# Kernel optimization log

Measured on AMD Instinct MI355X. Metric: run time of the kernel, lower is better.

Reference implementation:

```python
import jax, jax.numpy as jnp
import numpy as np

N = 100000      # nodes
E = 1600000     # edges (before self-loops)
IN = 256        # input features
HID = 128       # hidden channels
HEADS = 8
C = HID // HEADS  # per-head channels = 16
L = 3           # num GAT layers
EPS = 1e-5      # batchnorm eps
NEG_SLOPE = 0.2 # leaky relu slope (PyG GATConv default)


def setup_inputs() -> dict:
    key = jax.random.key(0)
    ks = jax.random.split(key, 8)
    s = 0.05
    x = jax.random.normal(ks[0], (N, IN), jnp.float32)
    edge_index = jax.random.randint(ks[1], (2, E), 0, N, dtype=jnp.int32)
    proj_w = jax.random.normal(ks[2], (IN, HID), jnp.float32) * s
    proj_b = jnp.zeros((HID,), jnp.float32)
    W = jax.random.normal(ks[3], (L, HID, HID), jnp.float32) * s
    att_src = jax.random.normal(ks[4], (L, HEADS, C), jnp.float32) * s
    att_dst = jax.random.normal(ks[5], (L, HEADS, C), jnp.float32) * s
    conv_b = jnp.zeros((L, HID), jnp.float32)
    bn_g = jnp.ones((L, HID), jnp.float32)
    bn_b = jnp.zeros((L, HID), jnp.float32)
    fc_w = jax.random.normal(ks[6], (HID, 1), jnp.float32) * s
    fc_b = jnp.zeros((1,), jnp.float32)
    return {"x": x, "edge_index": edge_index, "proj_w": proj_w, "proj_b": proj_b,
            "W": W, "att_src": att_src, "att_dst": att_dst, "conv_b": conv_b,
            "bn_g": bn_g, "bn_b": bn_b, "fc_w": fc_w, "fc_b": fc_b}


def _gat_layer(x, src, dst, W, a_src, a_dst, b):
    # x: [N, HID] -> per-head features h: [N, HEADS, C]
    h = (x @ W).reshape(N, HEADS, C)
    al_src = jnp.einsum('nhc,hc->nh', h, a_src)  # [N, HEADS]
    al_dst = jnp.einsum('nhc,hc->nh', h, a_dst)  # [N, HEADS]
    e = jax.nn.leaky_relu(al_src[src] + al_dst[dst], NEG_SLOPE)  # [Etot, HEADS]
    # segment softmax over edges grouped by destination node
    m = jax.ops.segment_max(e, dst, num_segments=N)              # [N, HEADS]
    w = jnp.exp(e - m[dst])
    denom = jax.ops.segment_sum(w, dst, num_segments=N)          # [N, HEADS]
    alpha = w / (denom[dst] + 1e-16)                             # [Etot, HEADS]
    msg = h[src] * alpha[:, :, None]                             # [Etot, HEADS, C]
    out = jax.ops.segment_sum(msg, dst, num_segments=N)          # [N, HEADS, C]
    return out.reshape(N, HID) + b


def reference(x, edge_index, proj_w, proj_b, W, att_src, att_dst, conv_b, bn_g, bn_b, fc_w, fc_b):
    # add self loops (PyG GATConv default)
    loops = jnp.arange(N, dtype=edge_index.dtype)
    src = jnp.concatenate([edge_index[0], loops])
    dst = jnp.concatenate([edge_index[1], loops])
    h = jax.nn.elu(x @ proj_w + proj_b)
    for i in range(L):
        res = h
        h = _gat_layer(h, src, dst, W[i], att_src[i], att_dst[i], conv_b[i])
        mu = h.mean(axis=0)
        var = h.var(axis=0)  # biased, matches torch BN training math
        h = (h - mu) / jnp.sqrt(var + EPS) * bn_g[i] + bn_b[i]
        h = jax.nn.elu(h)
        h = h + res  # residual; dropout is identity in eval mode
    return h @ fc_w + fc_b
```

## Files before the change

kernel.cpp:

```cpp
#include <hip/hip_runtime.h>
#include <hip/hip_bf16.h>

#define NN 100000
#define EE 1600000
#define ETOT (NN + EE)
#define HID 128
#define HEADS 8
#define CH 16
#define EPS_BN 1e-5f
#define NEG_SLOPE 0.2f
#define LOG2E 1.4426950408889634f
#define NB 196
#define NBLK_A 208

typedef unsigned short ushort_t;
typedef unsigned int uint_t;
typedef __attribute__((ext_vector_type(8))) short short8;
typedef __attribute__((ext_vector_type(4))) float float4v;

__device__ inline uint_t f2bf(float x) {
    __hip_bfloat16 b = __float2bfloat16(x);
    return (uint_t)*reinterpret_cast<unsigned short*>(&b);
}
__device__ inline uint_t pack2(float lo, float hi) {
    return f2bf(lo) | (f2bf(hi) << 16);
}
__device__ inline float bf_lo(uint_t u) { return __uint_as_float(u << 16); }
__device__ inline float bf_hi(uint_t u) { return __uint_as_float(u & 0xffff0000u); }

__device__ inline void gld_lds16(const void* g, void* l) {
    __builtin_amdgcn_global_load_lds(
        (const __attribute__((address_space(1))) unsigned int*)g,
        (__attribute__((address_space(3))) unsigned int*)l, 16, 0, 0);
}


__global__ __launch_bounds__(256) void bucket_hist(const int* __restrict__ ei,
                                                   int* bcnt, int* lbase) {
    __shared__ int h[256];
    int t = threadIdx.x;
    h[t] = 0;
    __syncthreads();
    int base = blockIdx.x * 8192;
    #pragma unroll 4
    for (int j = 0; j < 32; ++j) {
        int i = base + j * 256 + t;
        if (i < ETOT) {
            int d = (i < EE) ? ei[EE + i] : (i - EE);
            atomicAdd(&h[d >> 9], 1);
        }
    }
    __syncthreads();
    if (t < NB) {
        int v = h[t];
        lbase[blockIdx.x * NB + t] = v ? atomicAdd(&bcnt[t], v) : 0;
    }
}

__global__ void bucket_scan(const int* __restrict__ bcnt, int* bbase, int* rowptr) {
    __shared__ int s[256];
    int t = threadIdx.x;
    int orig = (t < NB) ? bcnt[t] : 0;
    s[t] = orig;
    __syncthreads();
    for (int off = 1; off < 256; off <<= 1) {
        int add = (t >= off) ? s[t - off] : 0;
        __syncthreads();
        s[t] += add;
        __syncthreads();
    }
    if (t < NB) bbase[t] = s[t] - orig;
    if (t == 0) { bbase[NB] = ETOT; rowptr[NN] = ETOT; }
}

__global__ __launch_bounds__(256) void bucket_scatter(const int* __restrict__ ei,
                                                      const int* __restrict__ bbase,
                                                      const int* __restrict__ lbase,
                                                      uint_t* __restrict__ pairs) {
    __shared__ uint_t spair[8192];
    __shared__ unsigned char sbk[8192];
    __shared__ int h[256];
    __shared__ int lscan[256];
    __shared__ int sbase[256];
    int t = threadIdx.x;
    int base = blockIdx.x * 8192;
    int nloc = ETOT - base; if (nloc > 8192) nloc = 8192;
    sbase[t] = (t < NB) ? (bbase[t] + lbase[blockIdx.x * NB + t]) : 0;
    h[t] = 0;
    __syncthreads();
    #pragma unroll 4
    for (int j = 0; j < 32; ++j) {
        int i = base + j * 256 + t;
        if (i < ETOT) {
            int d = (i < EE) ? ei[EE + i] : (i - EE);
            atomicAdd(&h[d >> 9], 1);
        }
    }
    __syncthreads();
    int orig = h[t];
    lscan[t] = orig;
    __syncthreads();
    for (int off = 1; off < 256; off <<= 1) {
        int add = (t >= off) ? lscan[t - off] : 0;
        __syncthreads();
        lscan[t] += add;
        __syncthreads();
    }
    int excl = lscan[t] - orig;
    __syncthreads();
    lscan[t] = excl;
    h[t] = excl;
    __syncthreads();
    #pragma unroll 4
    for (int j = 0; j < 32; ++j) {
        int i = base + j * 256 + t;
        if (i < ETOT) {
            int sv, dv;
            if (i < EE) { sv = ei[i]; dv = ei[EE + i]; }
            else        { sv = i - EE; dv = sv; }
            int bk = dv >> 9;
            int lp = atomicAdd(&h[bk], 1);
            spair[lp] = ((uint_t)sv << 9) | (uint_t)(dv & 511);
            sbk[lp] = (unsigned char)bk;
        }
    }
    __syncthreads();
    #pragma unroll 4
    for (int j = 0; j < 32; ++j) {
        int i = j * 256 + t;
        if (i < nloc) {
            int bk = sbk[i];
            pairs[sbase[bk] + (i - lscan[bk])] = spair[i];
        }
    }
}

__global__ __launch_bounds__(256) void bucket_build(const uint_t* __restrict__ pairs,
                                                    const int* __restrict__ bbase,
                                                    int* __restrict__ rowptr,
                                                    int* __restrict__ csrc) {
    __shared__ int cnt[512];
    __shared__ int cur[512];
    int b = blockIdx.x;
    int t = threadIdx.x;
    int lo = b << 9;
    int nn = NN - lo; if (nn > 512) nn = 512;
    int e0 = bbase[b];
    int e1 = bbase[b + 1];
    cnt[t] = 0; cnt[t + 256] = 0;
    __syncthreads();
    for (int i = e0 + t; i < e1; i += 256)
        atomicAdd(&cnt[pairs[i] & 511], 1);
    __syncthreads();
    int oc0 = cnt[t], oc1 = cnt[t + 256];
    for (int off = 1; off < 512; off <<= 1) {
        int i0 = t, i1 = t + 256;
        int a0 = cnt[i0] + ((i0 >= off) ? cnt[i0 - off] : 0);
        int a1 = cnt[i1] + ((i1 >= off) ? cnt[i1 - off] : 0);
        __syncthreads();
        cnt[i0] = a0; cnt[i1] = a1;
        __syncthreads();
    }
    int ex0 = cnt[t] - oc0, ex1 = cnt[t + 256] - oc1;
    __syncthreads();
    cur[t] = e0 + ex0; cur[t + 256] = e0 + ex1;
    if (t < nn)       rowptr[lo + t] = e0 + ex0;
    if (t + 256 < nn) rowptr[lo + 256 + t] = e0 + ex1;
    __syncthreads();
    for (int i = e0 + t; i < e1; i += 256) {
        uint_t p = pairs[i];
        int pos = atomicAdd(&cur[p & 511], 1);
        csrc[pos] = (int)(p >> 9);
    }
}


__global__ void castw(const float* __restrict__ proj_w, const float* __restrict__ W,
                      ushort_t* __restrict__ pwT, ushort_t* __restrict__ WT,
                      int* __restrict__ zbuf) {
    int id = blockIdx.x * 256 + threadIdx.x;
    if (id < 1024) zbuf[id] = 0;
    if (id < 32768) {
        int n = id >> 8, k = id & 255;
        pwT[id] = (ushort_t)f2bf(proj_w[k * 128 + n]);
    } else if (id < 81920) {
        int id2 = id - 32768;
        int l = id2 >> 14, r = id2 & 16383;
        int n = r >> 7, k = r & 127;
        WT[id2] = (ushort_t)f2bf(W[l * 16384 + k * 128 + n]);
    }
}


__global__ __launch_bounds__(512) void proj_gemm(
    const float* __restrict__ A, const ushort_t* __restrict__ Bt,
    const float* __restrict__ bias, ushort_t* __restrict__ Cb)
{
    __shared__ uint4 smem[4096];
    ushort_t* As = (ushort_t*)smem;
    ushort_t* Bs = As + 16384;

    int t = threadIdx.x;
    int row0 = blockIdx.x * 128;
    int lane = t & 63, wv = t >> 6;
    int wm = wv >> 1, wn = wv & 1;
    int lr = lane & 15, quad = lane >> 4;

    float4v acc[2][4] = {};

    for (int h = 0; h < 2; ++h) {
        #pragma unroll
        for (int j = 0; j < 4; ++j) {
            int idx = j * 512 + t;
            int tile = idx >> 8, ksf = (idx >> 6) & 3;
            int l = idx & 63;
            int n = tile * 16 + (l & 15);
            int kk = h * 128 + ksf * 32 + (l >> 4) * 8;
            gld_lds16(Bt + n * 256 + kk, Bs + (size_t)idx * 8);
        }
        #pragma unroll
        for (int j = 0; j < 4; ++j) {
            int idx = j * 512 + t;
            int tile = idx >> 8, ksf = (idx >> 6) & 3;
            int l = idx & 63;
            int row = row0 + tile * 16 + (l & 15);
            if (row >= NN) row = NN - 1;
            int kk = h * 128 + ksf * 32 + (l >> 4) * 8;
            const float* src = A + (size_t)row * 256 + kk;
            float4 v0 = *(const float4*)(src);
            float4 v1 = *(const float4*)(src + 4);
            uint4 o;
            o.x = pack2(v0.x, v0.y); o.y = pack2(v0.z, v0.w);
            o.z = pack2(v1.x, v1.y); o.w = pack2(v1.z, v1.w);
            *(uint4*)(As + (size_t)idx * 8) = o;
        }
        __syncthreads();

        #pragma unroll
        for (int ks = 0; ks < 4; ++ks) {
            short8 a[2], b[4];
            #pragma unroll
            for (int tj = 0; tj < 4; ++tj)
                b[tj] = *(const short8*)(Bs + ((wn * 4 + tj) * 4 + ks) * 512 + lane * 8);
            #pragma unroll
            for (int ti = 0; ti < 2; ++ti)
                a[ti] = *(const short8*)(As + ((wm * 2 + ti) * 4 + ks) * 512 + lane * 8);
            #pragma unroll
            for (int ti = 0; ti < 2; ++ti)
                #pragma unroll
                for (int tj = 0; tj < 4; ++tj)
                    acc[ti][tj] = __builtin_amdgcn_mfma_f32_16x16x32_bf16(
                        a[ti], b[tj], acc[ti][tj], 0, 0, 0);
        }
        __syncthreads();
    }

    float* sc = (float*)smem;
    for (int tp = 0; tp < 2; ++tp) {
        if ((wm >> 1) == tp) {
            #pragma unroll
            for (int ti = 0; ti < 2; ++ti) {
                #pragma unroll
                for (int tj = 0; tj < 4; ++tj) {
                    #pragma unroll
                    for (int r = 0; r < 4; ++r) {
                        int rloc = (wm & 1) * 32 + ti * 16 + quad * 4 + r;
                        int col = wn * 64 + tj * 16 + lr;
                        sc[rloc * 132 + col] = acc[ti][tj][r];
                    }
                }
            }
        }
        __syncthreads();
        #pragma unroll
        for (int j = 0; j < 4; ++j) {
            int idx = j * 512 + t;
            int row = idx >> 5;
            int c4 = (idx & 31) * 4;
            float4 v = *(const float4*)&sc[row * 132 + c4];
            int gr = row0 + tp * 64 + row;
            if (gr < NN) {
                float4 bv = *(const float4*)(bias + c4);
                v.x += bv.x; v.y += bv.y; v.z += bv.z; v.w += bv.w;
                v.x = v.x > 0.f ? v.x : __expf(v.x) - 1.f;
                v.y = v.y > 0.f ? v.y : __expf(v.y) - 1.f;
                v.z = v.z > 0.f ? v.z : __expf(v.z) - 1.f;
                v.w = v.w > 0.f ? v.w : __expf(v.w) - 1.f;
                uint2 u; u.x = pack2(v.x, v.y); u.y = pack2(v.z, v.w);
                *(uint2*)(Cb + (size_t)gr * 128 + c4) = u;
            }
        }
        __syncthreads();
    }
}


__global__ __launch_bounds__(512) void layer_gemm(
    const void* __restrict__ Aptr, int mode,
    const ushort_t* __restrict__ Bt, ushort_t* __restrict__ Cb,
    const float* __restrict__ a_src, const float* __restrict__ a_dst,
    float* __restrict__ al_s, float* __restrict__ al_d,
    uint_t* __restrict__ hbio, const float* __restrict__ stats,
    const float* __restrict__ bn_gl, const float* __restrict__ bn_bl)
{
    __shared__ uint4 smem[4096];
    __shared__ float2 scsh[128];
    ushort_t* As = (ushort_t*)smem;
    ushort_t* Bs = As + 16384;

    int t = threadIdx.x;
    int row0 = blockIdx.x * 128;
    int lane = t & 63, wv = t >> 6;
    int wm = wv >> 1, wn = wv & 1;
    int lr = lane & 15, quad = lane >> 4;

    if (mode == 2) {
        if (t < 128) {
            float mu = stats[t] * (1.0f / NN);
            float var = stats[128 + t] * (1.0f / NN) - mu * mu;
            float s = bn_gl[t] * rsqrtf(var + EPS_BN);
            scsh[t] = make_float2(s, bn_bl[t] - mu * s);
        }
        __syncthreads();
    }

    #pragma unroll
    for (int j = 0; j < 4; ++j) {
        int idx = j * 512 + t;
        int tile = idx >> 8, ksf = (idx >> 6) & 3;
        int l = idx & 63;
        int n = tile * 16 + (l & 15);
        int kk = ksf * 32 + (l >> 4) * 8;
        gld_lds16(Bt + n * 128 + kk, Bs + (size_t)idx * 8);
    }

    if (mode == 0) {
        const ushort_t* A = (const ushort_t*)Aptr;
        #pragma unroll
        for (int j = 0; j < 4; ++j) {
            int idx = j * 512 + t;
            int tile = idx >> 8, ksf = (idx >> 6) & 3;
            int l = idx & 63;
            int row = row0 + tile * 16 + (l & 15);
            int kk = ksf * 32 + (l >> 4) * 8;
            gld_lds16(A + (size_t)row * 128 + kk, As + (size_t)idx * 8);
        }
    } else {
        const uint_t* agg = (const uint_t*)Aptr;
        uint4 av[4], rv[4];
        unsigned gi[4];
        int rowv[4];
        #pragma unroll
        for (int j = 0; j < 4; ++j) {
            int idx = j * 512 + t;
            int tile = idx >> 8;
            int ksf = (idx >> 6) & 3;
            int l = idx & 63;
            int row = row0 + tile * 16 + (l & 15);
            int kk = ksf * 32 + (l >> 4) * 8;
            unsigned ui = (unsigned)row * 64u + (unsigned)(kk >> 1);
            gi[j] = ui; rowv[j] = row;
            av[j] = *(const uint4*)(agg + ui);
            rv[j] = *(const uint4*)(hbio + ui);
        }
        #pragma unroll
        for (int j = 0; j < 4; ++j) {
            int idx = j * 512 + t;
            int ksf = (idx >> 6) & 3;
            int l = idx & 63;
            int kk = ksf * 32 + (l >> 4) * 8;
            uint_t aa[4] = {av[j].x, av[j].y, av[j].z, av[j].w};
            uint_t rr[4] = {rv[j].x, rv[j].y, rv[j].z, rv[j].w};
            float ov[8];
            #pragma unroll
            for (int q = 0; q < 4; ++q) {
                float2 s0 = scsh[kk + 2 * q];
                float2 s1 = scsh[kk + 2 * q + 1];
                float x0 = s0.x * bf_lo(aa[q]) + s0.y;
                x0 = x0 > 0.f ? x0 : __expf(x0) - 1.f;
                x0 += bf_lo(rr[q]);
                float x1 = s1.x * bf_hi(aa[q]) + s1.y;
                x1 = x1 > 0.f ? x1 : __expf(x1) - 1.f;
                x1 += bf_hi(rr[q]);
                ov[2 * q] = x0; ov[2 * q + 1] = x1;
            }
            uint4 o;
            o.x = pack2(ov[0], ov[1]); o.y = pack2(ov[2], ov[3]);
            o.z = pack2(ov[4], ov[5]); o.w = pack2(ov[6], ov[7]);
            *(uint4*)(As + (size_t)idx * 8) = o;
            if (rowv[j] < NN) *(uint4*)(hbio + gi[j]) = o;
        }
    }
    __syncthreads();

    float4v acc[2][4] = {};
    #pragma unroll
    for (int ks = 0; ks < 4; ++ks) {
        short8 a[2], b[4];
        #pragma unroll
        for (int tj = 0; tj < 4; ++tj)
            b[tj] = *(const short8*)(Bs + ((wn * 4 + tj) * 4 + ks) * 512 + lane * 8);
        #pragma unroll
        for (int ti = 0; ti < 2; ++ti)
            a[ti] = *(const short8*)(As + ((wm * 2 + ti) * 4 + ks) * 512 + lane * 8);
        #pragma unroll
        for (int ti = 0; ti < 2; ++ti)
            #pragma unroll
            for (int tj = 0; tj < 4; ++tj)
                acc[ti][tj] = __builtin_amdgcn_mfma_f32_16x16x32_bf16(
                    a[ti], b[tj], acc[ti][tj], 0, 0, 0);
    }
    __syncthreads();

    float* sc = (float*)smem;
    for (int tp = 0; tp < 2; ++tp) {
        if ((wm >> 1) == tp) {
            #pragma unroll
            for (int ti = 0; ti < 2; ++ti) {
                #pragma unroll
                for (int tj = 0; tj < 4; ++tj) {
                    #pragma unroll
                    for (int r = 0; r < 4; ++r) {
                        int rloc = (wm & 1) * 32 + ti * 16 + quad * 4 + r;
                        int col = wn * 64 + tj * 16 + lr;
                        sc[rloc * 132 + col] = acc[ti][tj][r];
                    }
                }
            }
        }
        __syncthreads();
        #pragma unroll
        for (int j = 0; j < 4; ++j) {
            int idx = j * 512 + t;
            int row = idx >> 5;
            int c4 = (idx & 31) * 4;
            float4 v = *(const float4*)&sc[row * 132 + c4];
            int gr = row0 + tp * 64 + row;
            if (gr < NN) {
                uint2 u; u.x = pack2(v.x, v.y); u.y = pack2(v.z, v.w);
                *(uint2*)(Cb + (size_t)gr * 128 + c4) = u;
            }
        }
        {
            int row = t & 63, head = t >> 6;
            int gr = row0 + tp * 64 + row;
            if (gr < NN) {
                const float* rp = &sc[row * 132 + head * 16];
                const float* spv = a_src + head * 16;
                const float* dpv = a_dst + head * 16;
                float s1 = 0.f, s2 = 0.f;
                #pragma unroll
                for (int c = 0; c < 16; ++c) {
                    float hv = rp[c];
                    s1 += hv * spv[c];
                    s2 += hv * dpv[c];
                }
                al_s[gr * 8 + head] = s1 * LOG2E;
                al_d[gr * 8 + head] = s2 * LOG2E;
            }
        }
        __syncthreads();
    }
}


__global__ __launch_bounds__(256) void gat_agg(
    const int* __restrict__ rowptr, const int* __restrict__ csrc,
    const uint4* __restrict__ h2b4, const float* __restrict__ al_s,
    const float* __restrict__ al_d, const float* __restrict__ bias,
    uint4* __restrict__ out4)
{
    int wv = (blockIdx.x * blockDim.x + threadIdx.x) >> 6;
    int lane = threadIdx.x & 63;
    if (wv >= NN) return;
    int slot = lane >> 4;
    int ln = lane & 15;
    int head = ln >> 1;
    const char* hb8 = (const char*)h2b4;
    const char* as8 = (const char*)al_s;
    unsigned hoff = (unsigned)ln * 16u;
    unsigned aoff = (unsigned)head * 4u;
    int e0 = rowptr[wv], e1 = rowptr[wv + 1];
    float ald = al_d[(unsigned)wv * 8u + head];
    float ac[8] = {};
    float denom = 0.f;

    int e = e0;
    for (; e + 16 <= e1; e += 16) {
        int sA = csrc[e + slot];
        int sB = csrc[e + 4 + slot];
        int sC = csrc[e + 8 + slot];
        int sD = csrc[e + 12 + slot];
        float aA = *(const float*)(as8 + ((unsigned)sA * 32u + aoff));
        float aB = *(const float*)(as8 + ((unsigned)sB * 32u + aoff));
        float aC = *(const float*)(as8 + ((unsigned)sC * 32u + aoff));
        float aD = *(const float*)(as8 + ((unsigned)sD * 32u + aoff));
        uint4 pA = *(const uint4*)(hb8 + ((unsigned)sA * 256u + hoff));
        uint4 pB = *(const uint4*)(hb8 + ((unsigned)sB * 256u + hoff));
        uint4 pC = *(const uint4*)(hb8 + ((unsigned)sC * 256u + hoff));
        uint4 pD = *(const uint4*)(hb8 + ((unsigned)sD * 256u + hoff));
        float xA = aA + ald; xA = fmaxf(xA, NEG_SLOPE * xA); float wA = exp2f(xA);
        float xB = aB + ald; xB = fmaxf(xB, NEG_SLOPE * xB); float wB = exp2f(xB);
        float xC = aC + ald; xC = fmaxf(xC, NEG_SLOPE * xC); float wC = exp2f(xC);
        float xD = aD + ald; xD = fmaxf(xD, NEG_SLOPE * xD); float wD = exp2f(xD);
        uint_t uA[4] = {pA.x, pA.y, pA.z, pA.w};
        uint_t uB[4] = {pB.x, pB.y, pB.z, pB.w};
        uint_t uC[4] = {pC.x, pC.y, pC.z, pC.w};
        uint_t uD[4] = {pD.x, pD.y, pD.z, pD.w};
        #pragma unroll
        for (int q = 0; q < 4; ++q) {
            ac[2 * q]     += wA * bf_lo(uA[q]) + wB * bf_lo(uB[q])
                           + wC * bf_lo(uC[q]) + wD * bf_lo(uD[q]);
            ac[2 * q + 1] += wA * bf_hi(uA[q]) + wB * bf_hi(uB[q])
                           + wC * bf_hi(uC[q]) + wD * bf_hi(uD[q]);
        }
        denom += (wA + wB) + (wC + wD);
    }
    for (; e + 8 <= e1; e += 8) {
        int sA = csrc[e + slot];
        int sB = csrc[e + 4 + slot];
        float aA = *(const float*)(as8 + ((unsigned)sA * 32u + aoff));
        float aB = *(const float*)(as8 + ((unsigned)sB * 32u + aoff));
        uint4 pA = *(const uint4*)(hb8 + ((unsigned)sA * 256u + hoff));
        uint4 pB = *(const uint4*)(hb8 + ((unsigned)sB * 256u + hoff));
        float xA = aA + ald; xA = fmaxf(xA, NEG_SLOPE * xA);
        float wA = exp2f(xA);
        float xB = aB + ald; xB = fmaxf(xB, NEG_SLOPE * xB);
        float wB = exp2f(xB);
        uint_t uA[4] = {pA.x, pA.y, pA.z, pA.w};
        uint_t uB[4] = {pB.x, pB.y, pB.z, pB.w};
        #pragma unroll
        for (int q = 0; q < 4; ++q) {
            ac[2 * q]     += wA * bf_lo(uA[q]) + wB * bf_lo(uB[q]);
            ac[2 * q + 1] += wA * bf_hi(uA[q]) + wB * bf_hi(uB[q]);
        }
        denom += wA + wB;
    }
    for (; e < e1; e += 4) {
        int idx = e + slot;
        bool valid = idx < e1;
        int s = csrc[valid ? idx : e];
        float a = *(const float*)(as8 + ((unsigned)s * 32u + aoff));
        uint4 p = *(const uint4*)(hb8 + ((unsigned)s * 256u + hoff));
        float x = a + ald; x = fmaxf(x, NEG_SLOPE * x);
        float w = valid ? exp2f(x) : 0.f;
        uint_t u[4] = {p.x, p.y, p.z, p.w};
        #pragma unroll
        for (int q = 0; q < 4; ++q) {
            ac[2 * q]     += w * bf_lo(u[q]);
            ac[2 * q + 1] += w * bf_hi(u[q]);
        }
        denom += w;
    }
    #pragma unroll
    for (int q = 0; q < 8; ++q) {
        ac[q] += __shfl_xor(ac[q], 16, 64);
        ac[q] += __shfl_xor(ac[q], 32, 64);
    }
    denom += __shfl_xor(denom, 16, 64);
    denom += __shfl_xor(denom, 32, 64);
    if (slot == 0) {
        float inv = 1.0f / (denom + 1e-16f);
        int c = ln * 8;
        float4 b0 = *(const float4*)(bias + c);
        float4 b1 = *(const float4*)(bias + c + 4);
        uint4 o;
        o.x = pack2(ac[0] * inv + b0.x, ac[1] * inv + b0.y);
        o.y = pack2(ac[2] * inv + b0.z, ac[3] * inv + b0.w);
        o.z = pack2(ac[4] * inv + b1.x, ac[5] * inv + b1.y);
        o.w = pack2(ac[6] * inv + b1.z, ac[7] * inv + b1.w);
        out4[(size_t)wv * 16 + ln] = o;
    }
}


__global__ void bn_stats(const uint_t* __restrict__ ab, float* stats) {
    int t = threadIdx.x;
    int u_idx = t >> 1, hi = t & 1;
    float s = 0.f, q = 0.f;
    for (int r0 = blockIdx.x * 4; r0 < NN; r0 += gridDim.x * 4) {
        #pragma unroll
        for (int j = 0; j < 4; ++j) {
            int r = r0 + j;
            if (r < NN) {
                uint_t u = ab[(size_t)r * 64 + u_idx];
                float v = hi ? bf_hi(u) : bf_lo(u);
                s += v;
                q += v * v;
            }
        }
    }
    atomicAdd(&stats[t], s);
    atomicAdd(&stats[HID + t], q);
}


__global__ __launch_bounds__(256) void fc_fused(
    const uint_t* __restrict__ aggb, const uint_t* __restrict__ hb,
    const float* __restrict__ stats, const float* __restrict__ g,
    const float* __restrict__ be, const float* __restrict__ w,
    const float* __restrict__ fb, float* __restrict__ out)
{
    __shared__ float2 scsh[128];
    int t = threadIdx.x;
    if (t < 128) {
        float mu = stats[t] * (1.0f / NN);
        float var = stats[128 + t] * (1.0f / NN) - mu * mu;
        float s = g[t] * rsqrtf(var + EPS_BN);
        scsh[t] = make_float2(s, be[t] - mu * s);
    }
    __syncthreads();
    int wv = (blockIdx.x * 256 + t) >> 6;
    int lane = t & 63;
    if (wv >= NN) return;
    uint_t av = aggb[(size_t)wv * 64 + lane];
    uint_t rv = hb[(size_t)wv * 64 + lane];
    int c = lane * 2;
    float2 s0 = scsh[c], s1 = scsh[c + 1];
    float x0 = s0.x * bf_lo(av) + s0.y;
    x0 = x0 > 0.f ? x0 : __expf(x0) - 1.f;
    x0 += bf_lo(rv);
    float x1 = s1.x * bf_hi(av) + s1.y;
    x1 = x1 > 0.f ? x1 : __expf(x1) - 1.f;
    x1 += bf_hi(rv);
    float2 wl = *(const float2*)(w + c);
    float acc = x0 * wl.x + x1 * wl.y;
    #pragma unroll
    for (int off = 32; off > 0; off >>= 1)
        acc += __shfl_down(acc, off, 64);
    if (lane == 0) out[wv] = acc + fb[0];
}


extern "C" void kernel_launch(void* const* d_in, const int* in_sizes, int n_in,
                              void* d_out, int out_size, void* d_ws, size_t ws_size,
                              hipStream_t stream) {
    const float* x       = (const float*)d_in[0];
    const int*   ei      = (const int*)  d_in[1];
    const float* proj_w  = (const float*)d_in[2];
    const float* proj_b  = (const float*)d_in[3];
    const float* W       = (const float*)d_in[4];
    const float* att_src = (const float*)d_in[5];
    const float* att_dst = (const float*)d_in[6];
    const float* conv_b  = (const float*)d_in[7];
    const float* bn_g    = (const float*)d_in[8];
    const float* bn_b    = (const float*)d_in[9];
    const float* fc_w    = (const float*)d_in[10];
    const float* fc_b    = (const float*)d_in[11];
    float* out = (float*)d_out;

    char* p = (char*)d_ws;
    uint_t*   hb   = (uint_t*)p;   p += (size_t)NN * 64 * 4;
    uint_t*   h2b  = (uint_t*)p;   p += (size_t)NN * 64 * 4;
    uint_t*   aggb = (uint_t*)p;   p += (size_t)NN * 64 * 4;
    uint_t*   pairs = (uint_t*)aggb;
    float*    al_s = (float*)p;    p += (size_t)NN * HEADS * 4;
    float*    al_d = (float*)p;    p += (size_t)NN * HEADS * 4;
    int* rowptr    = (int*)p;      p += ((size_t)(NN + 1) * 4 + 255) & ~255ull;
    int* csrc      = (int*)p;      p += (size_t)ETOT * 4;
    int* bcnt      = (int*)p;      p += 1024;
    float* stats3  = (float*)p;    p += 3 * 1024;
    int* bbase     = (int*)p;      p += 1024;
    int* lbase     = (int*)p;      p += (size_t)NBLK_A * NB * 4 + 256;
    ushort_t* pwT  = (ushort_t*)p; p += 128 * 256 * 2;
    ushort_t* WT   = (ushort_t*)p; p += 3 * 128 * 128 * 2;
    (void)ws_size; (void)n_in; (void)in_sizes; (void)out_size;

    castw<<<320, 256, 0, stream>>>(proj_w, W, pwT, WT, bcnt);

    proj_gemm<<<(NN + 127) / 128, 512, 0, stream>>>(x, pwT, proj_b, (ushort_t*)hb);

    bucket_hist<<<NBLK_A, 256, 0, stream>>>(ei, bcnt, (int*)lbase);
    bucket_scan<<<1, 256, 0, stream>>>(bcnt, bbase, rowptr);
    bucket_scatter<<<NBLK_A, 256, 0, stream>>>(ei, bbase, (const int*)lbase, pairs);
    bucket_build<<<NB, 256, 0, stream>>>(pairs, bbase, rowptr, csrc);

    for (int l = 0; l < 3; ++l) {
        const ushort_t* WTl = WT + (size_t)l * 128 * 128;
        const float* asl = att_src + (size_t)l * HEADS * CH;
        const float* adl = att_dst + (size_t)l * HEADS * CH;
        const float* cbl = conv_b + (size_t)l * HID;
        float* stl = stats3 + l * 256;

        if (l == 0) {
            layer_gemm<<<(NN + 127) / 128, 512, 0, stream>>>(
                hb, 0, WTl, (ushort_t*)h2b, asl, adl, al_s, al_d,
                nullptr, nullptr, nullptr, nullptr);
        } else {
            layer_gemm<<<(NN + 127) / 128, 512, 0, stream>>>(
                aggb, 2, WTl, (ushort_t*)h2b, asl, adl, al_s, al_d,
                hb, stats3 + (l - 1) * 256, bn_g + (size_t)(l - 1) * HID,
                bn_b + (size_t)(l - 1) * HID);
        }
        gat_agg<<<(NN + 3) / 4, 256, 0, stream>>>(
            rowptr, csrc, (const uint4*)h2b, al_s, al_d, cbl, (uint4*)aggb);
        bn_stats<<<512, 128, 0, stream>>>(aggb, stl);
    }

    fc_fused<<<(NN + 3) / 4, 256, 0, stream>>>(
        aggb, hb, stats3 + 2 * 256, bn_g + 2 * HID, bn_b + 2 * HID, fc_w, fc_b, out);
}
```

Measured before the change: 774.4 us.

## Fuse batchnorm statistics into GAT aggregation with replicated partial sums

Removes the separate bn_stats kernel, which re-read the aggregated features after every layer. gat_agg now accumulates per-block sum and sum-of-squares in shared memory using LDS atomics, then adds them into one of 64 replicated global slots to spread atomic contention. The consumers (layer_gemm and fc_fused) reduce the 64 replicas before computing the BN scale and shift. This saves one full pass over the 100000x128 feature buffer per layer, at the cost of extra LDS atomics, two syncthreads per block and global atomics in the aggregation kernel.

```diff
diff --git a/kernel.cpp b/kernel.cpp
--- a/kernel.cpp
+++ b/kernel.cpp
@@ -12,6 +12,7 @@
 #define LOG2E 1.4426950408889634f
 #define NB 196
 #define NBLK_A 208
+#define SREP 64
 
 typedef unsigned short ushort_t;
 typedef unsigned int uint_t;
@@ -177,9 +178,10 @@
 
 __global__ void castw(const float* __restrict__ proj_w, const float* __restrict__ W,
                       ushort_t* __restrict__ pwT, ushort_t* __restrict__ WT,
-                      int* __restrict__ zbuf) {
+                      int* __restrict__ bcnt, float* __restrict__ srep) {
     int id = blockIdx.x * 256 + threadIdx.x;
-    if (id < 1024) zbuf[id] = 0;
+    if (id < 256) bcnt[id] = 0;
+    if (id < 3 * SREP * 256) srep[id] = 0.f;
     if (id < 32768) {
         int n = id >> 8, k = id & 255;
         pwT[id] = (ushort_t)f2bf(proj_w[k * 128 + n]);
@@ -300,7 +302,7 @@
     const ushort_t* __restrict__ Bt, ushort_t* __restrict__ Cb,
     const float* __restrict__ a_src, const float* __restrict__ a_dst,
     float* __restrict__ al_s, float* __restrict__ al_d,
-    uint_t* __restrict__ hbio, const float* __restrict__ stats,
+    uint_t* __restrict__ hbio, const float* __restrict__ srep,
     const float* __restrict__ bn_gl, const float* __restrict__ bn_bl)
 {
     __shared__ uint4 smem[4096];
@@ -316,8 +318,14 @@
 
     if (mode == 2) {
         if (t < 128) {
-            float mu = stats[t] * (1.0f / NN);
-            float var = stats[128 + t] * (1.0f / NN) - mu * mu;
+            float s_ = 0.f, q_ = 0.f;
+            #pragma unroll 8
+            for (int r = 0; r < SREP; ++r) {
+                s_ += srep[r * 256 + t];
+                q_ += srep[r * 256 + 128 + t];
+            }
+            float mu = s_ * (1.0f / NN);
+            float var = q_ * (1.0f / NN) - mu * mu;
             float s = bn_gl[t] * rsqrtf(var + EPS_BN);
             scsh[t] = make_float2(s, bn_bl[t] - mu * s);
         }
@@ -468,11 +476,15 @@
     const int* __restrict__ rowptr, const int* __restrict__ csrc,
     const uint4* __restrict__ h2b4, const float* __restrict__ al_s,
     const float* __restrict__ al_d, const float* __restrict__ bias,
-    uint4* __restrict__ out4)
+    uint4* __restrict__ out4, float* __restrict__ srep)
 {
-    int wv = (blockIdx.x * blockDim.x + threadIdx.x) >> 6;
-    int lane = threadIdx.x & 63;
-    if (wv >= NN) return;
+    __shared__ float ssum[256];
+    int tt = threadIdx.x;
+    ssum[tt] = 0.f;
+    __syncthreads();
+
+    int wv = (blockIdx.x * blockDim.x + tt) >> 6;
+    int lane = tt & 63;
     int slot = lane >> 4;
     int ln = lane & 15;
     int head = ln >> 1;
@@ -564,48 +576,45 @@
         int c = ln * 8;
         float4 b0 = *(const float4*)(bias + c);
         float4 b1 = *(const float4*)(bias + c + 4);
+        float v0 = ac[0] * inv + b0.x, v1 = ac[1] * inv + b0.y;
+        float v2 = ac[2] * inv + b0.z, v3 = ac[3] * inv + b0.w;
+        float v4 = ac[4] * inv + b1.x, v5 = ac[5] * inv + b1.y;
+        float v6 = ac[6] * inv + b1.z, v7 = ac[7] * inv + b1.w;
         uint4 o;
-        o.x = pack2(ac[0] * inv + b0.x, ac[1] * inv + b0.y);
-        o.y = pack2(ac[2] * inv + b0.z, ac[3] * inv + b0.w);
-        o.z = pack2(ac[4] * inv + b1.x, ac[5] * inv + b1.y);
-        o.w = pack2(ac[6] * inv + b1.z, ac[7] * inv + b1.w);
+        o.x = pack2(v0, v1); o.y = pack2(v2, v3);
+        o.z = pack2(v4, v5); o.w = pack2(v6, v7);
         out4[(size_t)wv * 16 + ln] = o;
-    }
-}
-
-
-__global__ void bn_stats(const uint_t* __restrict__ ab, float* stats) {
-    int t = threadIdx.x;
-    int u_idx = t >> 1, hi = t & 1;
-    float s = 0.f, q = 0.f;
-    for (int r0 = blockIdx.x * 4; r0 < NN; r0 += gridDim.x * 4) {
-        #pragma unroll
-        for (int j = 0; j < 4; ++j) {
-            int r = r0 + j;
-            if (r < NN) {
-                uint_t u = ab[(size_t)r * 64 + u_idx];
-                float v = hi ? bf_hi(u) : bf_lo(u);
-                s += v;
-                q += v * v;
-            }
-        }
-    }
-    atomicAdd(&stats[t], s);
-    atomicAdd(&stats[HID + t], q);
+        atomicAdd(&ssum[c + 0], v0);  atomicAdd(&ssum[128 + c + 0], v0 * v0);
+        atomicAdd(&ssum[c + 1], v1);  atomicAdd(&ssum[128 + c + 1], v1 * v1);
+        atomicAdd(&ssum[c + 2], v2);  atomicAdd(&ssum[128 + c + 2], v2 * v2);
+        atomicAdd(&ssum[c + 3], v3);  atomicAdd(&ssum[128 + c + 3], v3 * v3);
+        atomicAdd(&ssum[c + 4], v4);  atomicAdd(&ssum[128 + c + 4], v4 * v4);
+        atomicAdd(&ssum[c + 5], v5);  atomicAdd(&ssum[128 + c + 5], v5 * v5);
+        atomicAdd(&ssum[c + 6], v6);  atomicAdd(&ssum[128 + c + 6], v6 * v6);
+        atomicAdd(&ssum[c + 7], v7);  atomicAdd(&ssum[128 + c + 7], v7 * v7);
+    }
+    __syncthreads();
+    atomicAdd(&srep[(blockIdx.x & (SREP - 1)) * 256 + tt], ssum[tt]);
 }
 
 
 __global__ __launch_bounds__(256) void fc_fused(
     const uint_t* __restrict__ aggb, const uint_t* __restrict__ hb,
-    const float* __restrict__ stats, const float* __restrict__ g,
+    const float* __restrict__ srep, const float* __restrict__ g,
     const float* __restrict__ be, const float* __restrict__ w,
     const float* __restrict__ fb, float* __restrict__ out)
 {
     __shared__ float2 scsh[128];
     int t = threadIdx.x;
     if (t < 128) {
-        float mu = stats[t] * (1.0f / NN);
-        float var = stats[128 + t] * (1.0f / NN) - mu * mu;
+        float s_ = 0.f, q_ = 0.f;
+        #pragma unroll 8
+        for (int r = 0; r < SREP; ++r) {
+            s_ += srep[r * 256 + t];
+            q_ += srep[r * 256 + 128 + t];
+        }
+        float mu = s_ * (1.0f / NN);
+        float var = q_ * (1.0f / NN) - mu * mu;
         float s = g[t] * rsqrtf(var + EPS_BN);
         scsh[t] = make_float2(s, be[t] - mu * s);
     }
@@ -659,14 +668,14 @@
     int* rowptr    = (int*)p;      p += ((size_t)(NN + 1) * 4 + 255) & ~255ull;
     int* csrc      = (int*)p;      p += (size_t)ETOT * 4;
     int* bcnt      = (int*)p;      p += 1024;
-    float* stats3  = (float*)p;    p += 3 * 1024;
+    float* srep3   = (float*)p;    p += 3 * SREP * 256 * 4;
     int* bbase     = (int*)p;      p += 1024;
     int* lbase     = (int*)p;      p += (size_t)NBLK_A * NB * 4 + 256;
     ushort_t* pwT  = (ushort_t*)p; p += 128 * 256 * 2;
     ushort_t* WT   = (ushort_t*)p; p += 3 * 128 * 128 * 2;
     (void)ws_size; (void)n_in; (void)in_sizes; (void)out_size;
 
-    castw<<<320, 256, 0, stream>>>(proj_w, W, pwT, WT, bcnt);
+    castw<<<320, 256, 0, stream>>>(proj_w, W, pwT, WT, bcnt, srep3);
 
     proj_gemm<<<(NN + 127) / 128, 512, 0, stream>>>(x, pwT, proj_b, (ushort_t*)hb);
 
@@ -680,7 +689,7 @@
         const float* asl = att_src + (size_t)l * HEADS * CH;
         const float* adl = att_dst + (size_t)l * HEADS * CH;
         const float* cbl = conv_b + (size_t)l * HID;
-        float* stl = stats3 + l * 256;
+        float* srl = srep3 + (size_t)l * SREP * 256;
 
         if (l == 0) {
             layer_gemm<<<(NN + 127) / 128, 512, 0, stream>>>(
@@ -689,14 +698,14 @@
         } else {
             layer_gemm<<<(NN + 127) / 128, 512, 0, stream>>>(
                 aggb, 2, WTl, (ushort_t*)h2b, asl, adl, al_s, al_d,
-                hb, stats3 + (l - 1) * 256, bn_g + (size_t)(l - 1) * HID,
-                bn_b + (size_t)(l - 1) * HID);
-        }
-        gat_agg<<<(NN + 3) / 4, 256, 0, stream>>>(
-            rowptr, csrc, (const uint4*)h2b, al_s, al_d, cbl, (uint4*)aggb);
-        bn_stats<<<512, 128, 0, stream>>>(aggb, stl);
+                hb, srep3 + (size_t)(l - 1) * SREP * 256,
+                bn_g + (size_t)(l - 1) * HID, bn_b + (size_t)(l - 1) * HID);
+        }
+        gat_agg<<<NN / 4, 256, 0, stream>>>(
+            rowptr, csrc, (const uint4*)h2b, al_s, al_d, cbl, (uint4*)aggb, srl);
     }
 
     fc_fused<<<(NN + 3) / 4, 256, 0, stream>>>(
-        aggb, hb, stats3 + 2 * 256, bn_g + 2 * HID, bn_b + 2 * HID, fc_w, fc_b, out);
-}
+        aggb, hb, srep3 + 2 * (size_t)SREP * 256, bn_g + 2 * HID, bn_b + 2 * HID,
+        fc_w, fc_b, out);
+}
```

Result: slower. 887.8 us (+14.6%).
